# Performance work log

Measured on AMD Instinct MI355X. Metric: run time of the kernel, lower is better.

The kernel has to match this reference:

```python
import jax, jax.numpy as jnp
import numpy as np
import math

B, T, D, H = 4, 1024, 1024, 16
HD = D // H  # 64
ROPE_BASE = 10000.0


def _apply_rope(q, k):
    # q, k: [B, H, T, HD]; interleaved even/odd rotation as in RotaryEmbedding
    t_len = q.shape[2]
    half = q.shape[-1] // 2
    inv_freq = 1.0 / (ROPE_BASE ** (jnp.arange(half, dtype=jnp.float32) / half))
    freqs = jnp.arange(t_len, dtype=jnp.float32)[:, None] * inv_freq  # [T, half]
    cos = jnp.cos(freqs)
    sin = jnp.sin(freqs)

    def rot(u):
        u1 = u[..., ::2]   # even lanes
        u2 = u[..., 1::2]  # odd lanes
        e = u1 * cos - u2 * sin
        o = u2 * cos + u1 * sin
        return jnp.stack([e, o], axis=-1).reshape(u.shape)

    return rot(q), rot(k)


def _split_heads(x):
    b, t, d = x.shape
    return x.reshape(b, t, H, HD).transpose(0, 2, 1, 3)  # [B,H,T,HD]


def _mha(x, Wq, bq, Wk, bk, Wv, bv, Wo, bo, mask):
    q = _split_heads(jnp.einsum('btd,ed->bte', x, Wq) + bq)
    k = _split_heads(jnp.einsum('btd,ed->bte', x, Wk) + bk)
    v = _split_heads(jnp.einsum('btd,ed->bte', x, Wv) + bv)
    q, k = _apply_rope(q, k)
    scores = jnp.einsum('bhtd,bhsd->bhts', q.astype(jnp.float32),
                        k.astype(jnp.float32)) / math.sqrt(HD)
    scores = jnp.where(mask, scores, -jnp.inf)
    attn = jax.nn.softmax(scores, axis=-1).astype(v.dtype)
    ctx = jnp.einsum('bhts,bhsd->bhtd', attn.astype(jnp.float32),
                     v.astype(jnp.float32)).astype(v.dtype)
    ctx = ctx.transpose(0, 2, 1, 3).reshape(x.shape[0], x.shape[1], D)
    z = jnp.einsum('btd,ed->bte', ctx, Wo) + bo
    return z


def setup_inputs() -> dict:
    key = jax.random.key(0)
    ks = jax.random.split(key, 9)
    s = 0.02
    inp = {
        'x':  jax.random.normal(ks[0], (B, T, D), jnp.float32),
        'Wq': jax.random.normal(ks[1], (D, D), jnp.float32) * s,
        'bq': jax.random.normal(ks[2], (D,), jnp.float32) * s,
        'Wk': jax.random.normal(ks[3], (D, D), jnp.float32) * s,
        'bk': jax.random.normal(ks[4], (D,), jnp.float32) * s,
        'Wv': jax.random.normal(ks[5], (D, D), jnp.float32) * s,
        'bv': jax.random.normal(ks[6], (D,), jnp.float32) * s,
        'Wo': jax.random.normal(ks[7], (D, D), jnp.float32) * s,
        'bo': jax.random.normal(ks[8], (D,), jnp.float32) * s,
        'mask': jnp.tril(jnp.ones((T, T), dtype=bool))[None, None],  # causal
    }
    return inp


def reference(x, Wq, bq, Wk, bk, Wv, bv, Wo, bo, mask):
    return _mha(x, Wq, bq, Wk, bk, Wv, bv, Wo, bo, mask)
```

## Files before the change

### kernel.cpp

```cpp
#include <hip/hip_runtime.h>


#define T_SEQ 1024
#define NH    16
#define HDIM  64
#define DM    1024
#define MTOK  4096

typedef __attribute__((ext_vector_type(8))) short short8;
typedef __attribute__((ext_vector_type(4))) float f32x4;
typedef unsigned short u16;

__device__ __forceinline__ u16 f2bf(float f) {
  unsigned int u = __builtin_bit_cast(unsigned int, f);
  u += 0x7fffu + ((u >> 16) & 1u);
  return (u16)(u >> 16);
}

__device__ __forceinline__ void gll16(const void* g, void* l) {
  __builtin_amdgcn_global_load_lds(
      (const __attribute__((address_space(1))) unsigned int*)(unsigned long long)(g),
      (__attribute__((address_space(3))) unsigned int*)(unsigned int)(unsigned long long)(l),
      16, 0, 0);
}

__global__ void prep_kernel(const float* __restrict__ x,
                            const float* __restrict__ Wq, const float* __restrict__ Wk,
                            const float* __restrict__ Wv, const float* __restrict__ Wo,
                            u16* __restrict__ xb, u16* __restrict__ wall,
                            float* __restrict__ ctab, float* __restrict__ stab) {
  const int bid = blockIdx.x, tid = threadIdx.x;
  if (bid < 8192) {
    const float* src;
    u16* dst;
    int i;
    if (bid < 4096) {
      src = x; dst = xb; i = bid * 256 + tid;
    } else {
      const int w = (bid - 4096) >> 10;
      src = w == 0 ? Wq : w == 1 ? Wk : w == 2 ? Wv : Wo;
      dst = wall + (size_t)w * (DM * DM);
      i = ((bid - 4096) & 1023) * 256 + tid;
    }
    float4 f = ((const float4*)src)[i];
    unsigned long long pk = (unsigned long long)f2bf(f.x)
                          | ((unsigned long long)f2bf(f.y) << 16)
                          | ((unsigned long long)f2bf(f.z) << 32)
                          | ((unsigned long long)f2bf(f.w) << 48);
    ((unsigned long long*)dst)[i] = pk;
  } else {
    const int idx = (bid - 8192) * 256 + tid;
    const int t = idx >> 5, i = idx & 31;
    float inv = powf(10000.f, -(float)i * (1.0f / 32.0f));
    float f = (float)t * inv;
    ctab[idx] = cosf(f);
    stab[idx] = sinf(f);
  }
}

template<int BM, int BN, int AL, int BL, int MI, int NJ>
__device__ __forceinline__ void gemm_dbuf(
    const u16* __restrict__ A, const u16* __restrict__ Bw,
    int m0, int n0, u16* As, u16* Bs, f32x4 acc[MI][NJ]) {
  const int tid = threadIdx.x, lane = tid & 63, wave = tid >> 6;
  const int wr = wave >> 1, wc = wave & 1;
  const int NT = DM / 32;

  size_t aofs[AL], bofs[BL];
  int adst[AL], bdst[BL];
#pragma unroll
  for (int l = 0; l < AL; ++l) {
    const int idx = l * 256 + tid, r = idx >> 3, c = (idx & 7) ^ (r & 7);
    aofs[l] = (size_t)(m0 + 2 * r + (c >> 2)) * DM + (c & 3) * 8;
    adst[l] = idx * 8;
  }
#pragma unroll
  for (int l = 0; l < BL; ++l) {
    const int idx = l * 256 + tid, r = idx >> 3, c = (idx & 7) ^ (r & 7);
    bofs[l] = (size_t)(n0 + 2 * r + (c >> 2)) * DM + (c & 3) * 8;
    bdst[l] = idx * 8;
  }

#define STGD(t, b)                                                        \
  do {                                                                    \
    _Pragma("unroll") for (int l = 0; l < AL; ++l)                        \
      gll16(&A[aofs[l] + (t) * 32], &As[(b) * (BM * 32) + adst[l]]);      \
    _Pragma("unroll") for (int l = 0; l < BL; ++l)                        \
      gll16(&Bw[bofs[l] + (t) * 32], &Bs[(b) * (BN * 32) + bdst[l]]);     \
  } while (0)

  const int mrow = lane & 15, q = lane >> 4;
  int aoff[MI], boff[NJ];
#pragma unroll
  for (int i = 0; i < MI; ++i) {
    const int m = wr * (MI * 16) + i * 16 + mrow, r = m >> 1;
    const int p = (((m & 1) << 2) | q) ^ (r & 7);
    aoff[i] = r * 64 + p * 8;
  }
#pragma unroll
  for (int j = 0; j < NJ; ++j) {
    const int n = wc * (NJ * 16) + j * 16 + mrow, r = n >> 1;
    const int p = (((n & 1) << 2) | q) ^ (r & 7);
    boff[j] = r * 64 + p * 8;
  }

  STGD(0, 0);
  __syncthreads();
  for (int t = 0; t < NT; ++t) {
    if (t + 1 < NT) STGD(t + 1, (t + 1) & 1);
    const int boa = (t & 1) * (BM * 32), bob = (t & 1) * (BN * 32);
    short8 af[MI], bf[NJ];
#pragma unroll
    for (int i = 0; i < MI; ++i) af[i] = *(const short8*)&As[boa + aoff[i]];
#pragma unroll
    for (int j = 0; j < NJ; ++j) bf[j] = *(const short8*)&Bs[bob + boff[j]];
#pragma unroll
    for (int i = 0; i < MI; ++i)
#pragma unroll
      for (int j = 0; j < NJ; ++j)
        acc[i][j] = __builtin_amdgcn_mfma_f32_16x16x32_bf16(af[i], bf[j], acc[i][j], 0, 0, 0);
    __syncthreads();
  }
#undef STGD
}

__global__ __launch_bounds__(256, 3) void qkv_kernel(
    const u16* __restrict__ xb, const u16* __restrict__ wqkv,
    const float* __restrict__ bq, const float* __restrict__ bk, const float* __restrict__ bv,
    const float* __restrict__ ctab, const float* __restrict__ stab,
    u16* __restrict__ qbuf, u16* __restrict__ kbuf, u16* __restrict__ vt) {
  __shared__ __align__(16) u16 As[2 * 128 * 32];
  __shared__ __align__(16) u16 Bs[2 * 128 * 32];
  const int lin = blockIdx.x;
  const int swz = (lin & 7) * 96 + (lin >> 3);
  const int m0 = (swz / 24) * 128;
  const int n0 = (swz % 24) * 128;
  f32x4 acc[4][4];
#pragma unroll
  for (int i = 0; i < 4; ++i)
#pragma unroll
    for (int j = 0; j < 4; ++j)
#pragma unroll
      for (int r = 0; r < 4; ++r) acc[i][j][r] = 0.f;
  gemm_dbuf<128, 128, 2, 2, 4, 4>(xb, wqkv, m0, n0, As, Bs, acc);

  const int lane = threadIdx.x & 63, wave = threadIdx.x >> 6;
  const int wr = wave >> 1, wc = wave & 1;
  const int mode = n0 >> 10;
  const float* bias = mode == 0 ? bq : (mode == 1 ? bk : bv);
#pragma unroll
  for (int i = 0; i < 4; ++i) {
#pragma unroll
    for (int j = 0; j < 4; ++j) {
      const int e = n0 + wc * 64 + j * 16 + (lane & 15);
      const float bval = bias[e & 1023];
      const int h = (e >> 6) & 15, hd = e & 63;
#pragma unroll
      for (int r = 0; r < 4; ++r) {
        const int m = m0 + wr * 64 + i * 16 + ((lane >> 4) * 4) + r;
        const int b = m >> 10, t = m & 1023;
        float v = acc[i][j][r] + bval;
        if (mode < 2) {
          float p = __shfl_xor(v, 1);
          const int fi = hd >> 1;
          const float cc = ctab[t * 32 + fi], ss = stab[t * 32 + fi];
          v = (hd & 1) ? (v * cc + p * ss) : (v * cc - p * ss);
          u16* dst = mode == 0 ? qbuf : kbuf;
          dst[(((size_t)(b * NH + h) * T_SEQ + t) << 6) + hd] = f2bf(v);
        } else {
          vt[(((size_t)(b * NH + h) * HDIM + hd) << 10) + t] = f2bf(v);
        }
      }
    }
  }
}

__global__ __launch_bounds__(256) void attn_kernel(
    const u16* __restrict__ qbuf, const u16* __restrict__ kbuf,
    const u16* __restrict__ vtb, u16* __restrict__ ctx) {
  __shared__ __align__(16) u16 Ks[2][64 * 64];
  __shared__ __align__(16) u16 Vs[2][64 * 64];
  __shared__ __align__(16) u16 Psm[4][16 * 64];
  const int bh = blockIdx.x;
  const int b = bh >> 4, h = bh & 15;
  const int tid = threadIdx.x, lane = tid & 63, wave = tid >> 6;
  const u16* Qp = qbuf + (size_t)bh * T_SEQ * HDIM;
  const u16* Kp = kbuf + (size_t)bh * T_SEQ * HDIM;
  const u16* Vp = vtb + (size_t)bh * HDIM * T_SEQ;
  u16* Pw = &Psm[wave][0];

  const int srow = tid >> 3;
  const int schx = ((tid & 7) ^ (srow & 7)) * 8;
  const int lx = lane & 7;

#define STG(kvt, bb)                                                            \
  do {                                                                          \
    _Pragma("unroll") for (int c = 0; c < 2; ++c) {                             \
      const int rr = c * 32 + srow;                                             \
      gll16(&Kp[(kvt) * 4096 + rr * 64 + schx], &Ks[bb][c * 2048 + tid * 8]);   \
      gll16(&Vp[(size_t)rr * T_SEQ + (kvt) * 64 + schx], &Vs[bb][c * 2048 + tid * 8]); \
    }                                                                           \
  } while (0)

  for (int phase = 0; phase < 2; ++phase) {
    const int qt = phase ? (15 - (int)blockIdx.y) : (int)blockIdx.y;
    const int q0 = qt * 64;
    const int nkv = qt + 1;
    const int qrow = q0 + wave * 16 + (lane & 15);
    const short8 qf0 = *(const short8*)&Qp[qrow * 64 + ((lane >> 4) * 8)];
    const short8 qf1 = *(const short8*)&Qp[qrow * 64 + 32 + ((lane >> 4) * 8)];

    f32x4 acc_o[4];
    float m_r[4], l_r[4];
#pragma unroll
    for (int i = 0; i < 4; ++i) {
#pragma unroll
      for (int r = 0; r < 4; ++r) acc_o[i][r] = 0.f;
      m_r[i] = -__builtin_inff();
      l_r[i] = 0.f;
    }

    __syncthreads();
    STG(0, 0);
    int cur = 0;

    for (int kvt = 0; kvt < nkv; ++kvt) {
      __syncthreads();
      if (kvt + 1 < nkv) STG(kvt + 1, cur ^ 1);

      f32x4 sacc[4];
#pragma unroll
      for (int cb = 0; cb < 4; ++cb) {
#pragma unroll
        for (int r = 0; r < 4; ++r) sacc[cb][r] = 0.f;
        const int krow = cb * 16 + (lane & 15);
        const short8 kf0 = *(const short8*)&Ks[cur][krow * 64 + (((lane >> 4) ^ lx) * 8)];
        const short8 kf1 = *(const short8*)&Ks[cur][krow * 64 + (((4 + (lane >> 4)) ^ lx) * 8)];
        sacc[cb] = __builtin_amdgcn_mfma_f32_16x16x32_bf16(qf0, kf0, sacc[cb], 0, 0, 0);
        sacc[cb] = __builtin_amdgcn_mfma_f32_16x16x32_bf16(qf1, kf1, sacc[cb], 0, 0, 0);
      }
      const int trow_base = q0 + wave * 16 + ((lane >> 4) * 4);
#pragma unroll
      for (int cb = 0; cb < 4; ++cb) {
        const int scol = kvt * 64 + cb * 16 + (lane & 15);
#pragma unroll
        for (int r = 0; r < 4; ++r) {
          float sv = sacc[cb][r] * 0.125f;
          sacc[cb][r] = (scol > trow_base + r) ? -__builtin_inff() : sv;
        }
      }
      float mt[4];
#pragma unroll
      for (int r = 0; r < 4; ++r)
        mt[r] = fmaxf(fmaxf(sacc[0][r], sacc[1][r]), fmaxf(sacc[2][r], sacc[3][r]));
#pragma unroll
      for (int off = 1; off < 16; off <<= 1)
#pragma unroll
        for (int r = 0; r < 4; ++r) mt[r] = fmaxf(mt[r], __shfl_xor(mt[r], off));
      float sf[4], lt[4];
#pragma unroll
      for (int r = 0; r < 4; ++r) {
        const float mn = fmaxf(m_r[r], mt[r]);
        sf[r] = __expf(m_r[r] - mn);
        m_r[r] = mn;
        lt[r] = 0.f;
      }
#pragma unroll
      for (int cb = 0; cb < 4; ++cb)
#pragma unroll
        for (int r = 0; r < 4; ++r) {
          const float p = __expf(sacc[cb][r] - m_r[r]);
          sacc[cb][r] = p;
          lt[r] += p;
        }
#pragma unroll
      for (int off = 1; off < 16; off <<= 1)
#pragma unroll
        for (int r = 0; r < 4; ++r) lt[r] += __shfl_xor(lt[r], off);
#pragma unroll
      for (int r = 0; r < 4; ++r) l_r[r] = l_r[r] * sf[r] + lt[r];
#pragma unroll
      for (int hb = 0; hb < 4; ++hb)
#pragma unroll
        for (int r = 0; r < 4; ++r) acc_o[hb][r] *= sf[r];

#pragma unroll
      for (int cb = 0; cb < 4; ++cb)
#pragma unroll
        for (int r = 0; r < 4; ++r) {
          const int prow = (lane >> 4) * 4 + r;
          Pw[prow * 64 + ((cb * 16 + (lane & 15)) ^ ((prow & 7) << 3))] = f2bf(sacc[cb][r]);
        }

      const int prr = lane & 15;
#pragma unroll
      for (int kc = 0; kc < 2; ++kc) {
        const short8 pf = *(const short8*)&Pw[prr * 64 + (((kc * 4 + (lane >> 4)) ^ lx) * 8)];
#pragma unroll
        for (int hb = 0; hb < 4; ++hb) {
          const int vrow = hb * 16 + (lane & 15);
          const short8 vf = *(const short8*)&Vs[cur][vrow * 64 + (((kc * 4 + (lane >> 4)) ^ lx) * 8)];
          acc_o[hb] = __builtin_amdgcn_mfma_f32_16x16x32_bf16(pf, vf, acc_o[hb], 0, 0, 0);
        }
      }
      cur ^= 1;
    }

#pragma unroll
    for (int hb = 0; hb < 4; ++hb) {
      const int hd = hb * 16 + (lane & 15);
#pragma unroll
      for (int r = 0; r < 4; ++r) {
        const int t = q0 + wave * 16 + ((lane >> 4) * 4) + r;
        const float v = acc_o[hb][r] / l_r[r];
        ctx[((size_t)(b * T_SEQ + t) * NH + h) * HDIM + hd] = f2bf(v);
      }
    }
  }
#undef STG
}

__global__ __launch_bounds__(256, 2) void oproj_kernel(
    const u16* __restrict__ ctx, const u16* __restrict__ Wob,
    const float* __restrict__ bo, float* __restrict__ out) {
  __shared__ __align__(16) u16 As[2 * 64 * 32];
  __shared__ __align__(16) u16 Bs[2 * 128 * 32];
  const int lin = blockIdx.x;
  const int swz = (lin & 7) * 64 + (lin >> 3);
  const int m0 = (swz / 8) * 64;
  const int n0 = (swz % 8) * 128;
  f32x4 acc[2][4];
#pragma unroll
  for (int i = 0; i < 2; ++i)
#pragma unroll
    for (int j = 0; j < 4; ++j)
#pragma unroll
      for (int r = 0; r < 4; ++r) acc[i][j][r] = 0.f;
  gemm_dbuf<64, 128, 1, 2, 2, 4>(ctx, Wob, m0, n0, As, Bs, acc);
  const int lane = threadIdx.x & 63, wave = threadIdx.x >> 6;
  const int wr = wave >> 1, wc = wave & 1;
#pragma unroll
  for (int i = 0; i < 2; ++i)
#pragma unroll
    for (int j = 0; j < 4; ++j) {
      const int e = n0 + wc * 64 + j * 16 + (lane & 15);
      const float bval = bo[e];
#pragma unroll
      for (int r = 0; r < 4; ++r) {
        const int m = m0 + wr * 32 + i * 16 + ((lane >> 4) * 4) + r;
        out[(size_t)m * DM + e] = acc[i][j][r] + bval;
      }
    }
}

extern "C" void kernel_launch(void* const* d_in, const int* in_sizes, int n_in,
                              void* d_out, int out_size, void* d_ws, size_t ws_size,
                              hipStream_t stream) {
  const float* x  = (const float*)d_in[0];
  const float* Wq = (const float*)d_in[1];
  const float* bq = (const float*)d_in[2];
  const float* Wk = (const float*)d_in[3];
  const float* bk = (const float*)d_in[4];
  const float* Wv = (const float*)d_in[5];
  const float* bv = (const float*)d_in[6];
  const float* Wo = (const float*)d_in[7];
  const float* bo = (const float*)d_in[8];

  char* w = (char*)d_ws;
  u16* xb   = (u16*)(w);
  u16* wall = (u16*)(w + (8ull << 20));
  u16* wob  = (u16*)(w + (14ull << 20));
  u16* qb   = (u16*)(w + (16ull << 20));
  u16* kb   = (u16*)(w + (24ull << 20));
  u16* vtb  = (u16*)(w + (32ull << 20));
  u16* ctxb = (u16*)(w + (40ull << 20));
  float* ctab = (float*)(w + (48ull << 20));
  float* stab = ctab + T_SEQ * 32;

  prep_kernel<<<dim3(8192 + 128), 256, 0, stream>>>(x, Wq, Wk, Wv, Wo, xb, wall, ctab, stab);
  qkv_kernel<<<dim3(768), 256, 0, stream>>>(
      xb, wall, bq, bk, bv, ctab, stab, qb, kb, vtb);
  attn_kernel<<<dim3(64, 8), 256, 0, stream>>>(qb, kb, vtb, ctxb);
  oproj_kernel<<<dim3(512), 256, 0, stream>>>(ctxb, wob, bo, (float*)d_out);
}
```

Baseline: 115.4 us.

## Rewrite QKV GEMM with 256x256 tiles, 8 waves, and 4-stage LDS pipeline

Replaces the 128x128 double-buffered QKV projection GEMM with a 256x256-tile kernel using 512 threads and 128 KB of dynamic LDS. Loads are staged four half-k-tiles ahead with global_load_lds, and MFMA bursts are interleaved with barriers and s_setprio to overlap loads with compute. The aim is more operand reuse per block and better latency hiding. In exchange it uses only 192 blocks at one block per CU, which may underfill the GPU, and it carries heavier register pressure from 32 accumulators per thread.

```diff
diff --git a/kernel.cpp b/kernel.cpp
--- a/kernel.cpp
+++ b/kernel.cpp
@@ -58,6 +58,163 @@
   }
 }
 
+__global__ __launch_bounds__(512, 1) void qkv_kernel(
+    const u16* __restrict__ xb, const u16* __restrict__ wqkv,
+    const float* __restrict__ bq, const float* __restrict__ bk, const float* __restrict__ bv,
+    const float* __restrict__ ctab, const float* __restrict__ stab,
+    u16* __restrict__ qbuf, u16* __restrict__ kbuf, u16* __restrict__ vt) {
+  extern __shared__ __align__(16) u16 smem[];
+  u16* As = smem;
+  u16* Bs = smem + 32768;
+
+  const int tid = threadIdx.x, lane = tid & 63, wave = tid >> 6;
+  const int wr = wave >> 2, wc = wave & 3;
+  const int lin = blockIdx.x;
+  const int swz = (lin & 7) * 24 + (lin >> 3);
+  const int m0 = (swz & 15) * 256;
+  const int n0 = (swz >> 4) * 256;
+
+  int adst[2];
+  size_t aofs[2], bofs[2];
+#pragma unroll
+  for (int l = 0; l < 2; ++l) {
+    const int idx = l * 512 + tid, lr = idx >> 3, lc = (idx & 7) ^ (lr & 7);
+    const int row = lr * 2 + (lc >> 2), ko = (lc & 3) * 8;
+    adst[l] = idx * 8;
+    aofs[l] = (size_t)(m0 + row) * DM + ko;
+    bofs[l] = (size_t)(n0 + row) * DM + ko;
+  }
+  auto stgA = [&](int kt, int kh) {
+#pragma unroll
+    for (int l = 0; l < 2; ++l)
+      gll16(&xb[aofs[l] + kt * 64 + kh * 32], &As[((kt & 1) * 2 + kh) * 8192 + adst[l]]);
+  };
+  auto stgB = [&](int kt, int kh) {
+#pragma unroll
+    for (int l = 0; l < 2; ++l)
+      gll16(&wqkv[bofs[l] + kt * 64 + kh * 32], &Bs[((kt & 1) * 2 + kh) * 8192 + adst[l]]);
+  };
+
+  int aoff[2][4], boff[4];
+#pragma unroll
+  for (int mh = 0; mh < 2; ++mh)
+#pragma unroll
+    for (int i = 0; i < 4; ++i) {
+      const int m = wr * 128 + mh * 64 + i * 16 + (lane & 15), lr = m >> 1;
+      const int pc = (((m & 1) << 2) | (lane >> 4)) ^ (lr & 7);
+      aoff[mh][i] = lr * 64 + pc * 8;
+    }
+#pragma unroll
+  for (int jn = 0; jn < 4; ++jn) {
+    const int n = wc * 64 + jn * 16 + (lane & 15), lr = n >> 1;
+    const int pc = (((n & 1) << 2) | (lane >> 4)) ^ (lr & 7);
+    boff[jn] = lr * 64 + pc * 8;
+  }
+
+  f32x4 acc[8][4];
+#pragma unroll
+  for (int i = 0; i < 8; ++i)
+#pragma unroll
+    for (int j = 0; j < 4; ++j)
+#pragma unroll
+      for (int r = 0; r < 4; ++r) acc[i][j][r] = 0.f;
+
+  short8 af[4], bf[4];
+  auto rdA = [&](const u16* base, int mh) {
+#pragma unroll
+    for (int i = 0; i < 4; ++i) af[i] = *(const short8*)&base[aoff[mh][i]];
+  };
+  auto rdB = [&](const u16* base) {
+#pragma unroll
+    for (int jn = 0; jn < 4; ++jn) bf[jn] = *(const short8*)&base[boff[jn]];
+  };
+
+#define MM(mb)                                                                       \
+  do {                                                                               \
+    __builtin_amdgcn_s_setprio(1);                                                   \
+    _Pragma("unroll") for (int i = 0; i < 4; ++i)                                    \
+      _Pragma("unroll") for (int jn = 0; jn < 4; ++jn)                               \
+        acc[(mb) + i][jn] =                                                          \
+            __builtin_amdgcn_mfma_f32_16x16x32_bf16(af[i], bf[jn], acc[(mb) + i][jn], 0, 0, 0); \
+    __builtin_amdgcn_s_setprio(0);                                                   \
+  } while (0)
+#define BAR __builtin_amdgcn_s_barrier()
+#define SGB __builtin_amdgcn_sched_barrier(0)
+
+  stgA(0, 0); stgB(0, 0); stgA(0, 1); stgB(0, 1); stgA(1, 0); stgB(1, 0);
+  asm volatile("s_waitcnt vmcnt(4)" ::: "memory");
+  BAR; SGB;
+
+#pragma unroll 1
+  for (int it = 0; it < 8; ++it) {
+    const int b = 2 * it + 1, c = 2 * it + 2, d = 2 * it + 3;
+    const bool full = (it < 7);
+    rdB(Bs + 0); rdA(As + 0, 0);
+    stgA(b, 1);
+    BAR; MM(0); BAR;
+    rdA(As + 0, 1);
+    stgB(b, 1);
+    BAR; MM(4); BAR;
+    rdB(Bs + 8192); rdA(As + 8192, 0);
+    if (full) stgA(c, 0);
+    BAR; MM(0); BAR;
+    rdA(As + 8192, 1);
+    if (full) {
+      stgB(c, 0);
+      asm volatile("s_waitcnt vmcnt(4)" ::: "memory");
+    } else {
+      asm volatile("s_waitcnt vmcnt(0)" ::: "memory");
+    }
+    BAR; SGB; MM(4); BAR;
+    rdB(Bs + 16384); rdA(As + 16384, 0);
+    if (full) stgA(c, 1);
+    BAR; MM(0); BAR;
+    rdA(As + 16384, 1);
+    if (full) stgB(c, 1);
+    BAR; MM(4); BAR;
+    rdB(Bs + 24576); rdA(As + 24576, 0);
+    if (full) stgA(d, 0);
+    BAR; MM(0); BAR;
+    rdA(As + 24576, 1);
+    if (full) {
+      stgB(d, 0);
+      asm volatile("s_waitcnt vmcnt(4)" ::: "memory");
+    }
+    BAR; SGB; MM(4); BAR;
+  }
+#undef MM
+#undef BAR
+#undef SGB
+
+  const int mode = n0 >> 10;
+  const float* bias = mode == 0 ? bq : (mode == 1 ? bk : bv);
+#pragma unroll
+  for (int mi = 0; mi < 8; ++mi) {
+#pragma unroll
+    for (int nj = 0; nj < 4; ++nj) {
+      const int e = n0 + wc * 64 + nj * 16 + (lane & 15);
+      const float bval = bias[e & 1023];
+      const int h = (e >> 6) & 15, hd = e & 63;
+#pragma unroll
+      for (int r = 0; r < 4; ++r) {
+        const int m = m0 + wr * 128 + mi * 16 + ((lane >> 4) * 4) + r;
+        const int bb = m >> 10, t = m & 1023;
+        float v = acc[mi][nj][r] + bval;
+        if (mode < 2) {
+          float p = __shfl_xor(v, 1);
+          const int fi = hd >> 1;
+          const float cc = ctab[t * 32 + fi], ss = stab[t * 32 + fi];
+          v = (hd & 1) ? (v * cc + p * ss) : (v * cc - p * ss);
+          u16* dst = mode == 0 ? qbuf : kbuf;
+          dst[(((size_t)(bb * NH + h) * T_SEQ + t) << 6) + hd] = f2bf(v);
+        } else {
+          vt[(((size_t)(bb * NH + h) * HDIM + hd) << 10) + t] = f2bf(v);
+        }
+      }
+    }
+  }
+}
+
 template<int BM, int BN, int AL, int BL, int MI, int NJ>
 __device__ __forceinline__ void gemm_dbuf(
     const u16* __restrict__ A, const u16* __restrict__ Bw,
@@ -122,57 +279,6 @@
     __syncthreads();
   }
 #undef STGD
-}
-
-__global__ __launch_bounds__(256, 3) void qkv_kernel(
-    const u16* __restrict__ xb, const u16* __restrict__ wqkv,
-    const float* __restrict__ bq, const float* __restrict__ bk, const float* __restrict__ bv,
-    const float* __restrict__ ctab, const float* __restrict__ stab,
-    u16* __restrict__ qbuf, u16* __restrict__ kbuf, u16* __restrict__ vt) {
-  __shared__ __align__(16) u16 As[2 * 128 * 32];
-  __shared__ __align__(16) u16 Bs[2 * 128 * 32];
-  const int lin = blockIdx.x;
-  const int swz = (lin & 7) * 96 + (lin >> 3);
-  const int m0 = (swz / 24) * 128;
-  const int n0 = (swz % 24) * 128;
-  f32x4 acc[4][4];
-#pragma unroll
-  for (int i = 0; i < 4; ++i)
-#pragma unroll
-    for (int j = 0; j < 4; ++j)
-#pragma unroll
-      for (int r = 0; r < 4; ++r) acc[i][j][r] = 0.f;
-  gemm_dbuf<128, 128, 2, 2, 4, 4>(xb, wqkv, m0, n0, As, Bs, acc);
-
-  const int lane = threadIdx.x & 63, wave = threadIdx.x >> 6;
-  const int wr = wave >> 1, wc = wave & 1;
-  const int mode = n0 >> 10;
-  const float* bias = mode == 0 ? bq : (mode == 1 ? bk : bv);
-#pragma unroll
-  for (int i = 0; i < 4; ++i) {
-#pragma unroll
-    for (int j = 0; j < 4; ++j) {
-      const int e = n0 + wc * 64 + j * 16 + (lane & 15);
-      const float bval = bias[e & 1023];
-      const int h = (e >> 6) & 15, hd = e & 63;
-#pragma unroll
-      for (int r = 0; r < 4; ++r) {
-        const int m = m0 + wr * 64 + i * 16 + ((lane >> 4) * 4) + r;
-        const int b = m >> 10, t = m & 1023;
-        float v = acc[i][j][r] + bval;
-        if (mode < 2) {
-          float p = __shfl_xor(v, 1);
-          const int fi = hd >> 1;
-          const float cc = ctab[t * 32 + fi], ss = stab[t * 32 + fi];
-          v = (hd & 1) ? (v * cc + p * ss) : (v * cc - p * ss);
-          u16* dst = mode == 0 ? qbuf : kbuf;
-          dst[(((size_t)(b * NH + h) * T_SEQ + t) << 6) + hd] = f2bf(v);
-        } else {
-          vt[(((size_t)(b * NH + h) * HDIM + hd) << 10) + t] = f2bf(v);
-        }
-      }
-    }
-  }
 }
 
 __global__ __launch_bounds__(256) void attn_kernel(
@@ -377,8 +483,11 @@
   float* ctab = (float*)(w + (48ull << 20));
   float* stab = ctab + T_SEQ * 32;
 
+  hipFuncSetAttribute(reinterpret_cast<const void*>(qkv_kernel),
+                      hipFuncAttributeMaxDynamicSharedMemorySize, 131072);
+
   prep_kernel<<<dim3(8192 + 128), 256, 0, stream>>>(x, Wq, Wk, Wv, Wo, xb, wall, ctab, stab);
-  qkv_kernel<<<dim3(768), 256, 0, stream>>>(
+  qkv_kernel<<<dim3(192), 512, 131072, stream>>>(
       xb, wall, bq, bk, bv, ctab, stab, qb, kb, vtb);
   attn_kernel<<<dim3(64, 8), 256, 0, stream>>>(qb, kb, vtb, ctxb);
   oproj_kernel<<<dim3(512), 256, 0, stream>>>(ctxb, wob, bo, (float*)d_out);
```

Measured after the change: 136.5 us. +18.2%, slower.
